# Kernel tuning notes

Measured on AMD Instinct MI355X. Metric: run time of the kernel, lower is better.

Reference implementation:

```python
import jax, jax.numpy as jnp
import numpy as np

L, V, D, S_MAX, B, S, H = 8, 32000, 1024, 1024, 4, 1024, 16
FF = 4 * D
EPS = 1e-5


def setup_inputs() -> dict:
    key = jax.random.key(0)
    ks = jax.random.split(key, 20)
    g = lambda k, shape: jax.random.normal(k, shape, dtype=jnp.float32) * 0.02
    inp = {
        'tokens': jax.random.randint(ks[0], (B, S), 0, V, dtype=jnp.int32),
        'num_heads': H,
        'emb': g(ks[1], (V, D)),
        'pos_emb': g(ks[2], (S_MAX, D)),
        'Wq': g(ks[3], (L, D, D)), 'bq': jnp.zeros((L, D), jnp.float32),
        'Wk': g(ks[4], (L, D, D)), 'bk': jnp.zeros((L, D), jnp.float32),
        'Wv': g(ks[5], (L, D, D)), 'bv': jnp.zeros((L, D), jnp.float32),
        'Wo': g(ks[6], (L, D, D)), 'bo': jnp.zeros((L, D), jnp.float32),
        'n1_s': jnp.ones((L, D), jnp.float32), 'n1_b': jnp.zeros((L, D), jnp.float32),
        'W1': g(ks[7], (L, D, FF)), 'b1': jnp.zeros((L, FF), jnp.float32),
        'W2': g(ks[8], (L, FF, D)), 'b2': jnp.zeros((L, D), jnp.float32),
        'n2_s': jnp.ones((L, D), jnp.float32), 'n2_b': jnp.zeros((L, D), jnp.float32),
    }
    return inp


def _layernorm(x, s, b):
    mu = jnp.mean(x, axis=-1, keepdims=True)
    var = jnp.mean(jnp.square(x - mu), axis=-1, keepdims=True)
    return s * (x - mu) * jax.lax.rsqrt(var + EPS) + b


def _forward(tokens, num_heads, emb, pos_emb, Wq, bq, Wk, bk, Wv, bv, Wo, bo,
             n1_s, n1_b, W1, b1, W2, b2, n2_s, n2_b):
    Bn, Sn = tokens.shape
    d = emb.shape[1]
    hd = d // num_heads
    x = emb[tokens] + pos_emb[:Sn][None, :, :]  # [B,S,D]

    def split_heads(t):  # [B,S,D] -> [B,H,S,hd]
        return t.reshape(Bn, Sn, num_heads, hd).transpose(0, 2, 1, 3)

    causal = jnp.triu(jnp.ones((Sn, Sn), dtype=bool), k=1)
    scale = 1.0 / np.sqrt(hd)
    nlayers = Wq.shape[0]
    for l in range(nlayers):
        q = split_heads(x @ Wq[l] + bq[l])
        k = split_heads(x @ Wk[l] + bk[l])
        v = split_heads(x @ Wv[l] + bv[l])
        scores = jnp.einsum('bhqd,bhkd->bhqk', q, k) * scale
        scores = jnp.where(causal, -jnp.inf, scores)
        attn = jax.nn.softmax(scores, axis=-1)
        ctx = jnp.einsum('bhqk,bhkd->bhqd', attn, v)
        ctx = ctx.transpose(0, 2, 1, 3).reshape(Bn, Sn, d)
        x = _layernorm(x + (ctx @ Wo[l] + bo[l]), n1_s[l], n1_b[l])
        h = jax.nn.relu(x @ W1[l] + b1[l])
        x = _layernorm(x + (h @ W2[l] + b2[l]), n2_s[l], n2_b[l])
    return x @ emb.T  # tied output head -> [B,S,V]


def reference(tokens, num_heads, emb, pos_emb, Wq, bq, Wk, bk, Wv, bv, Wo, bo,
              n1_s, n1_b, W1, b1, W2, b2, n2_s, n2_b):
    return _forward(tokens, num_heads, emb, pos_emb, Wq, bq, Wk, bk, Wv, bv,
                    Wo, bo, n1_s, n1_b, W1, b1, W2, b2, n2_s, n2_b)
```

## Files before the change

### kernel.cpp

```cpp
#include <hip/hip_runtime.h>

#define D_MODEL 1024
#define SEQ     1024
#define BATCH   4
#define NHEAD   16
#define HDIM    64
#define FF_DIM  4096
#define NLAYER  8
#define VOCAB   32000
#define ROWS    (BATCH*SEQ)
#define QKV_N   3072
#define LN_EPS  1e-5f

typedef __attribute__((ext_vector_type(4))) float   f32x4;
typedef __attribute__((ext_vector_type(8))) unsigned short u16x8;
typedef __attribute__((ext_vector_type(8))) __bf16  bf16x8;

typedef const unsigned int __attribute__((address_space(1)))* gas_t;
typedef unsigned int __attribute__((address_space(3)))* las_t;

__device__ __forceinline__ void gld16(const void* g, void* l) {
    __builtin_amdgcn_global_load_lds((gas_t)g, (las_t)l, 16, 0, 0);
}

__device__ __forceinline__ unsigned short f2bf(float f) {
    unsigned int u = __builtin_bit_cast(unsigned int, f);
    u += 0x7FFFu + ((u >> 16) & 1u);
    return (unsigned short)(u >> 16);
}

__device__ __forceinline__ float bf2f(unsigned short u) {
    return __builtin_bit_cast(float, (unsigned int)u << 16);
}

__device__ __forceinline__ f32x4 mfma32(u16x8 a, u16x8 b, f32x4 c) {
    return __builtin_amdgcn_mfma_f32_16x16x32_bf16(
        __builtin_bit_cast(bf16x8, a), __builtin_bit_cast(bf16x8, b), c, 0, 0, 0);
}

__global__ __launch_bounds__(256) void embed_k(
    const int* __restrict__ tok, const float* __restrict__ emb,
    const float* __restrict__ pos, float* __restrict__ x,
    unsigned short* __restrict__ xb)
{
    int bs = blockIdx.x;
    int s  = bs & (SEQ - 1);
    int tk = tok[bs];
    int c  = threadIdx.x * 4;
    float4 e = *(const float4*)(emb + (size_t)tk * D_MODEL + c);
    float4 p = *(const float4*)(pos + (size_t)s * D_MODEL + c);
    float y0 = e.x + p.x, y1 = e.y + p.y, y2 = e.z + p.z, y3 = e.w + p.w;
    size_t base = (size_t)bs * D_MODEL + c;
    *(float4*)(x + base) = make_float4(y0, y1, y2, y3);
    unsigned long long pk = (unsigned long long)f2bf(y0)
        | ((unsigned long long)f2bf(y1) << 16)
        | ((unsigned long long)f2bf(y2) << 32)
        | ((unsigned long long)f2bf(y3) << 48);
    *(unsigned long long*)(xb + base) = pk;
}

__global__ __launch_bounds__(256) void cast_bf(
    const float* __restrict__ in, unsigned short* __restrict__ out, size_t n)
{
    size_t i = ((size_t)blockIdx.x * 256 + threadIdx.x) * 4;
    if (i >= n) return;
    float4 v = *(const float4*)(in + i);
    unsigned long long pk = (unsigned long long)f2bf(v.x)
        | ((unsigned long long)f2bf(v.y) << 16)
        | ((unsigned long long)f2bf(v.z) << 32)
        | ((unsigned long long)f2bf(v.w) << 48);
    *(unsigned long long*)(out + i) = pk;
}

__global__ __launch_bounds__(256) void bias3_k(
    const float* __restrict__ bq, const float* __restrict__ bk,
    const float* __restrict__ bv, float* __restrict__ out)
{
    int l = blockIdx.x / 3, which = blockIdx.x % 3;
    const float* src = which == 0 ? bq : (which == 1 ? bk : bv);
    int i = threadIdx.x * 4;
    float4 v = *(const float4*)(src + (size_t)l * D_MODEL + i);
    *(float4*)(out + (size_t)l * QKV_N + which * D_MODEL + i) = v;
}

__device__ __forceinline__ void tc_tile(
    const float* __restrict__ W, unsigned short* __restrict__ Wt,
    int K, int N, int n0, int k0)
{
    __shared__ float t[64][65];
    int rr = threadIdx.x >> 4;
    int cc = (threadIdx.x & 15) * 4;
#pragma unroll
    for (int it = 0; it < 4; it++) {
        int r = it * 16 + rr;
        float4 v = *(const float4*)(W + (size_t)(k0 + r) * N + n0 + cc);
        t[r][cc] = v.x; t[r][cc + 1] = v.y; t[r][cc + 2] = v.z; t[r][cc + 3] = v.w;
    }
    __syncthreads();
#pragma unroll
    for (int it = 0; it < 4; it++) {
        int n = it * 16 + rr;
        unsigned long long pk = (unsigned long long)f2bf(t[cc][n])
            | ((unsigned long long)f2bf(t[cc + 1][n]) << 16)
            | ((unsigned long long)f2bf(t[cc + 2][n]) << 32)
            | ((unsigned long long)f2bf(t[cc + 3][n]) << 48);
        *(unsigned long long*)(Wt + (size_t)(n0 + n) * K + k0 + cc) = pk;
    }
}

__global__ __launch_bounds__(256) void transpose_cast(
    const float* __restrict__ W, unsigned short* __restrict__ Wt, int K, int N)
{
    tc_tile(W, Wt, K, N, blockIdx.x * 64, blockIdx.y * 64);
}

__global__ __launch_bounds__(256) void transpose_cast3(
    const float* __restrict__ Wq, const float* __restrict__ Wk,
    const float* __restrict__ Wv, unsigned short* __restrict__ Wt)
{
    const int which = blockIdx.z;
    const float* W = which == 0 ? Wq : (which == 1 ? Wk : Wv);
    tc_tile(W, Wt + (size_t)which * (1024 * 1024), 1024, 1024,
            blockIdx.x * 64, blockIdx.y * 64);
}

__global__ __launch_bounds__(256) void transpose_all(
    const float* __restrict__ Wq, const float* __restrict__ Wk,
    const float* __restrict__ Wv, const float* __restrict__ Wo,
    const float* __restrict__ W1, const float* __restrict__ W2,
    unsigned short* __restrict__ wt)
{
    int b = blockIdx.x;
    const float* W; unsigned short* out; int K, N, t;
    if (b < 768)       { int w = b >> 8; t = b & 255; W = w == 0 ? Wq : (w == 1 ? Wk : Wv);
                         out = wt + (size_t)w * 1048576; K = 1024; N = 1024; }
    else if (b < 1024) { t = b - 768;  W = Wo; out = wt + (size_t)3 * 1048576; K = 1024; N = 1024; }
    else if (b < 2048) { t = b - 1024; W = W1; out = wt + (size_t)4 * 1048576; K = 1024; N = 4096; }
    else               { t = b - 2048; W = W2; out = wt + (size_t)8 * 1048576; K = 4096; N = 1024; }
    int ntx = N >> 6;
    tc_tile(W, out, K, N, (t % ntx) * 64, (t / ntx) * 64);
}

template<int MODE>
__global__ __launch_bounds__(256, 3) void gemm_bt(
    const unsigned short* __restrict__ A, int lda,
    const unsigned short* __restrict__ Bt, int ldb,
    const float* __restrict__ bias, void* __restrict__ Cout, int N, int Klen)
{
    __shared__ unsigned short As[128 * 32];
    __shared__ unsigned short Bs[128 * 32];
    const int part = blockIdx.y;
    A  += (size_t)part * Klen;
    Bt += (size_t)part * Klen;
    int flat = blockIdx.x;
    const int bm = flat & 31, bn = flat >> 5;
    const int tid  = threadIdx.x;
    const int wid  = tid >> 6, lane = tid & 63;
    const int l16  = lane & 15, lhi = lane >> 4;
    const int wr   = wid >> 1, wc = wid & 1;

    const int srow = wid * 32 + (lane >> 2);
    const int scol = (lane & 3) * 8;
    const unsigned short* gA0 = A  + ((size_t)bm * 128 + srow) * lda + scol;
    const unsigned short* gB0 = Bt + ((size_t)bn * 128 + srow) * ldb + scol;
    unsigned short* lA = As + wid * 32 * 32;
    unsigned short* lB = Bs + wid * 32 * 32;

    f32x4 acc[4][4];
#pragma unroll
    for (int i = 0; i < 4; i++)
#pragma unroll
        for (int j = 0; j < 4; j++) acc[i][j] = (f32x4){0.f, 0.f, 0.f, 0.f};

    for (int k0 = 0; k0 < Klen; k0 += 32) {
        __syncthreads();
        gld16(gA0 + k0,                    lA);
        gld16(gA0 + k0 + 16 * (size_t)lda, lA + 16 * 32);
        gld16(gB0 + k0,                    lB);
        gld16(gB0 + k0 + 16 * (size_t)ldb, lB + 16 * 32);
        __syncthreads();
        u16x8 af[4], bfr[4];
#pragma unroll
        for (int i = 0; i < 4; i++)
            af[i] = *(const u16x8*)(As + (wr * 64 + i * 16 + l16) * 32 + lhi * 8);
#pragma unroll
        for (int i = 0; i < 4; i++)
            bfr[i] = *(const u16x8*)(Bs + (wc * 64 + i * 16 + l16) * 32 + lhi * 8);
#pragma unroll
        for (int mi = 0; mi < 4; mi++)
#pragma unroll
            for (int ni = 0; ni < 4; ni++)
                acc[mi][ni] = mfma32(af[mi], bfr[ni], acc[mi][ni]);
    }

    const size_t pofs = (size_t)part * (size_t)ROWS * N;
#pragma unroll
    for (int mi = 0; mi < 4; mi++)
#pragma unroll
        for (int ni = 0; ni < 4; ni++) {
            int row = bm * 128 + wr * 64 + mi * 16 + lhi * 4;
            int col = bn * 128 + wc * 64 + ni * 16 + l16;
            float bv = (bias && part == 0) ? bias[col] : 0.f;
#pragma unroll
            for (int j = 0; j < 4; j++) {
                float v = acc[mi][ni][j] + bv;
                size_t idx = pofs + (size_t)(row + j) * N + col;
                if constexpr (MODE == 1) {
                    ((unsigned short*)Cout)[idx] = f2bf(v);
                } else {
                    ((unsigned short*)Cout)[idx] = f2bf(v > 0.f ? v : 0.f);
                }
            }
        }
}

#define PSYNC() do { __builtin_amdgcn_s_barrier(); \
    asm volatile("s_waitcnt lgkmcnt(0)" ::: "memory"); \
    __builtin_amdgcn_sched_barrier(0); } while (0)
#define PEND() __builtin_amdgcn_s_barrier()
#define VM4()  asm volatile("s_waitcnt vmcnt(4)" ::: "memory")

#define LOADA(reg, half) do { \
    _Pragma("unroll") \
    for (int m_ = 0; m_ < 4; m_++) { \
        aF[m_][0] = *(const u16x8*)((reg) + ((half)*4 + m_) * 2048 + lane0); \
        aF[m_][1] = *(const u16x8*)((reg) + ((half)*4 + m_) * 2048 + lane1); \
    } } while (0)

#define LOADB(reg, np) do { \
    _Pragma("unroll") \
    for (int n_ = 0; n_ < 2; n_++) { \
        bF[(np)*2 + n_][0] = *(const u16x8*)((reg) + ((np)*2 + n_) * 2048 + lane0); \
        bF[(np)*2 + n_][1] = *(const u16x8*)((reg) + ((np)*2 + n_) * 2048 + lane1); \
    } } while (0)

#define MFMA8(ma, np) do { \
    __builtin_amdgcn_s_setprio(1); \
    _Pragma("unroll") \
    for (int m_ = 0; m_ < 4; m_++) \
        _Pragma("unroll") \
        for (int n_ = 0; n_ < 2; n_++) { \
            acc[(ma)+m_][(np)*2+n_] = mfma32(aF[m_][0], bF[(np)*2+n_][0], acc[(ma)+m_][(np)*2+n_]); \
            acc[(ma)+m_][(np)*2+n_] = mfma32(aF[m_][1], bF[(np)*2+n_][1], acc[(ma)+m_][(np)*2+n_]); \
        } \
    __builtin_amdgcn_s_setprio(0); \
} while (0)

template<int MODE, int SWZ>
__global__ __launch_bounds__(512, 2) void gemm256(
    const unsigned short* __restrict__ A, const unsigned short* __restrict__ Bt,
    const float* __restrict__ bias, void* __restrict__ Cout, int N, int K)
{
    __shared__ unsigned short lds[65536] __attribute__((aligned(128)));
    const int tid = threadIdx.x, wid = tid >> 6, lane = tid & 63;
    const int l16 = lane & 15, lhi = lane >> 4;
    const int wr = wid >> 2, wc = wid & 3;

    int flat = blockIdx.x;
    if constexpr (SWZ) {
        int cpx = gridDim.x >> 3; flat = (flat & 7) * cpx + (flat >> 3);
    }
    const int bm = flat & 15, bn = flat >> 4;
    const int NT = K >> 6;

    const int srowL = tid >> 3;
    const int scolb = ((tid & 7) << 4) ^ (((tid >> 3) & 7) << 4);
    const unsigned short* baseA = A  + (size_t)(bm * 256 + srowL) * K + (scolb >> 1);
    const unsigned short* baseB = Bt + (size_t)(bn * 256 + srowL) * K + (scolb >> 1);
    unsigned short* dst0 = lds + wid * 512;

    auto stage = [&](int isB, int tile, int h) {
        const unsigned short* s = (isB ? baseB : baseA) + (size_t)(h * 128) * K + (size_t)tile * 64;
        unsigned short* d = dst0 + (tile & 1) * 32768 + isB * 16384 + h * 8192;
        gld16(s, d);
        gld16(s + (size_t)64 * K, d + 4096);
    };

    const int lswz  = (l16 & 7) << 4;
    const int lane0 = ((lhi * 16) ^ lswz) + l16 * 128;
    const int lane1 = ((64 + lhi * 16) ^ lswz) + l16 * 128;

    const char* aR0 = (const char*)lds + wr * 16384;
    const char* bR0 = (const char*)lds + 32768 + (wc >> 1) * 16384 + (wc & 1) * 8192;
    const char* aR1 = aR0 + 65536;
    const char* bR1 = bR0 + 65536;

    f32x4 acc[8][4];
#pragma unroll
    for (int i = 0; i < 8; i++)
#pragma unroll
        for (int j = 0; j < 4; j++) acc[i][j] = (f32x4){0.f, 0.f, 0.f, 0.f};
    u16x8 aF[4][2], bF[4][2];

    stage(1, 0, 0); stage(1, 0, 1);
    stage(0, 0, 0); stage(0, 0, 1);
    stage(1, 1, 0); stage(1, 1, 1);
    VM4();
    __builtin_amdgcn_s_barrier();

    for (int t = 0; t < NT; t += 2) {
        const bool more = (t + 2) < NT;
        LOADA(aR0, 0); LOADB(bR0, 0); stage(0, t + 1, 0);
        PSYNC(); MFMA8(0, 0); PEND();
        LOADB(bR0, 1);                stage(0, t + 1, 1);
        PSYNC(); MFMA8(0, 1); PEND();
        LOADA(aR0, 1);                if (more) stage(1, t + 2, 0);
        PSYNC(); MFMA8(4, 0); PEND();
        if (more) { stage(1, t + 2, 1); VM4(); }
        else      { asm volatile("s_waitcnt vmcnt(0)" ::: "memory"); }
        PSYNC(); MFMA8(4, 1); PEND();
        LOADA(aR1, 0); LOADB(bR1, 0); if (more) stage(0, t + 2, 0);
        PSYNC(); MFMA8(0, 0); PEND();
        LOADB(bR1, 1);                if (more) stage(0, t + 2, 1);
        PSYNC(); MFMA8(0, 1); PEND();
        LOADA(aR1, 1);                if (more) stage(1, t + 3, 0);
        PSYNC(); MFMA8(4, 0); PEND();
        if (more) { stage(1, t + 3, 1); VM4(); }
        PSYNC(); MFMA8(4, 1); PEND();
    }

#pragma unroll
    for (int mi = 0; mi < 8; mi++)
#pragma unroll
        for (int ni = 0; ni < 4; ni++) {
            int row = bm * 256 + wr * 128 + mi * 16 + lhi * 4;
            int col = bn * 256 + wc * 64 + ni * 16 + l16;
            float bv = bias ? bias[col] : 0.f;
#pragma unroll
            for (int j = 0; j < 4; j++) {
                float v = acc[mi][ni][j] + bv;
                size_t idx = (size_t)(row + j) * N + col;
                if constexpr (MODE == 0) {
                    __builtin_nontemporal_store(v, (float*)Cout + idx);
                } else if constexpr (MODE == 1) {
                    ((unsigned short*)Cout)[idx] = f2bf(v);
                } else {
                    ((unsigned short*)Cout)[idx] = f2bf(v > 0.f ? v : 0.f);
                }
            }
        }
}

__global__ __launch_bounds__(256, 3) void attn_fwd(
    const unsigned short* __restrict__ qkv, unsigned short* __restrict__ ctxb)
{
    __shared__ unsigned short Ks[64 * 72];
    __shared__ unsigned short Vs[64 * 72];
    __shared__ unsigned short Ps[4 * 16 * 72];
    const int tid = threadIdx.x;
    const int wid = tid >> 6, lane = tid & 63;
    const int l16 = lane & 15, lhi = lane >> 4;
    const int bh  = blockIdx.y, b = bh >> 4, h = bh & 15;
    const int q0  = blockIdx.x * 64;
    const size_t rowbase = (size_t)b * SEQ;

    const int qrow = q0 + wid * 16 + l16;
    const unsigned short* qp = qkv + (rowbase + qrow) * QKV_N + h * HDIM + lhi * 8;
    u16x8 qf0 = *(const u16x8*)qp;
    u16x8 qf1 = *(const u16x8*)(qp + 32);

    f32x4 oa[4];
    float mj[4], lj[4];
#pragma unroll
    for (int i = 0; i < 4; i++) {
        oa[i] = (f32x4){0.f, 0.f, 0.f, 0.f};
        mj[i] = -1e30f; lj[i] = 0.f;
    }

    const int ntiles = blockIdx.x + 1;
    for (int kt = 0; kt < ntiles; ++kt) {
        const int kv0 = kt * 64;
        __syncthreads();
#pragma unroll
        for (int it = 0; it < 2; ++it) {
            int e = it * 256 + tid;
            int r = e >> 3, d0 = (e & 7) * 8;
            size_t goff = (rowbase + kv0 + r) * QKV_N + D_MODEL + h * HDIM + d0;
            u16x8 kk = *(const u16x8*)(qkv + goff);
            *(u16x8*)(&Ks[r * 72 + d0]) = kk;
        }
        if (tid < 128) {
            int r0 = (tid & 15) * 4, d0v = (tid >> 4) * 8;
            const unsigned short* vp = qkv + (rowbase + kv0 + r0) * QKV_N
                                       + 2 * D_MODEL + h * HDIM + d0v;
            u16x8 w0 = *(const u16x8*)vp;
            u16x8 w1 = *(const u16x8*)(vp + QKV_N);
            u16x8 w2 = *(const u16x8*)(vp + 2 * QKV_N);
            u16x8 w3 = *(const u16x8*)(vp + 3 * QKV_N);
#pragma unroll
            for (int j = 0; j < 8; j++) {
                unsigned long long pk = (unsigned long long)w0[j]
                    | ((unsigned long long)w1[j] << 16)
                    | ((unsigned long long)w2[j] << 32)
                    | ((unsigned long long)w3[j] << 48);
                *(unsigned long long*)(&Vs[(d0v + j) * 72 + r0]) = pk;
            }
        }
        __syncthreads();

        f32x4 sa[4];
#pragma unroll
        for (int ni = 0; ni < 4; ni++) {
            f32x4 z = (f32x4){0.f, 0.f, 0.f, 0.f};
            u16x8 k0f = *(const u16x8*)(&Ks[(ni * 16 + l16) * 72 + lhi * 8]);
            u16x8 k1f = *(const u16x8*)(&Ks[(ni * 16 + l16) * 72 + 32 + lhi * 8]);
            z = mfma32(qf0, k0f, z);
            z = mfma32(qf1, k1f, z);
            sa[ni] = z;
        }
        float tm[4] = {-1e30f, -1e30f, -1e30f, -1e30f};
#pragma unroll
        for (int ni = 0; ni < 4; ni++)
#pragma unroll
            for (int j = 0; j < 4; j++) {
                float v = sa[ni][j] * 0.125f;
                int row = q0 + wid * 16 + lhi * 4 + j;
                int col = kv0 + ni * 16 + l16;
                if (col > row) v = -1e30f;
                sa[ni][j] = v;
                tm[j] = fmaxf(tm[j], v);
            }
#pragma unroll
        for (int j = 0; j < 4; j++) {
#pragma unroll
            for (int off = 1; off < 16; off <<= 1)
                tm[j] = fmaxf(tm[j], __shfl_xor(tm[j], off));
        }
        float al[4], rs[4] = {0.f, 0.f, 0.f, 0.f};
#pragma unroll
        for (int j = 0; j < 4; j++) {
            float mn = fmaxf(mj[j], tm[j]);
            al[j] = __expf(mj[j] - mn);
            mj[j] = mn;
        }
#pragma unroll
        for (int ni = 0; ni < 4; ni++)
#pragma unroll
            for (int j = 0; j < 4; j++) {
                float p = __expf(sa[ni][j] - mj[j]);
                rs[j] += p;
                Ps[wid * 1152 + (lhi * 4 + j) * 72 + ni * 16 + l16] = f2bf(p);
            }
#pragma unroll
        for (int j = 0; j < 4; j++) {
#pragma unroll
            for (int off = 1; off < 16; off <<= 1)
                rs[j] += __shfl_xor(rs[j], off);
            lj[j] = lj[j] * al[j] + rs[j];
        }
#pragma unroll
        for (int di = 0; di < 4; di++)
#pragma unroll
            for (int j = 0; j < 4; j++) oa[di][j] *= al[j];
#pragma unroll
        for (int di = 0; di < 4; di++) {
#pragma unroll
            for (int kc = 0; kc < 2; kc++) {
                u16x8 pf = *(const u16x8*)(&Ps[wid * 1152 + l16 * 72 + kc * 32 + lhi * 8]);
                u16x8 vf = *(const u16x8*)(&Vs[(di * 16 + l16) * 72 + kc * 32 + lhi * 8]);
                oa[di] = mfma32(pf, vf, oa[di]);
            }
        }
    }
#pragma unroll
    for (int di = 0; di < 4; di++)
#pragma unroll
        for (int j = 0; j < 4; j++) {
            int row = q0 + wid * 16 + lhi * 4 + j;
            ctxb[(rowbase + row) * D_MODEL + h * HDIM + di * 16 + l16] =
                f2bf(oa[di][j] / lj[j]);
        }
}

__global__ __launch_bounds__(256) void ln3(
    float* __restrict__ x, const unsigned short* __restrict__ p0,
    const unsigned short* __restrict__ p1,
    const float* __restrict__ sc, const float* __restrict__ bi,
    unsigned short* __restrict__ xb)
{
    const int row = blockIdx.x;
    const int t = threadIdx.x;
    const size_t base = (size_t)row * D_MODEL + t * 4;
    float4 xv = *(const float4*)(x + base);
    ushort4 au = *(const ushort4*)(p0 + base);
    ushort4 bu = *(const ushort4*)(p1 + base);
    float v0 = xv.x + bf2f(au.x) + bf2f(bu.x);
    float v1 = xv.y + bf2f(au.y) + bf2f(bu.y);
    float v2 = xv.z + bf2f(au.z) + bf2f(bu.z);
    float v3 = xv.w + bf2f(au.w) + bf2f(bu.w);
    float sum = v0 + v1 + v2 + v3;
    float sq  = v0 * v0 + v1 * v1 + v2 * v2 + v3 * v3;
#pragma unroll
    for (int off = 1; off < 64; off <<= 1) {
        sum += __shfl_xor(sum, off);
        sq  += __shfl_xor(sq, off);
    }
    __shared__ float red[8];
    int wid = t >> 6, lane = t & 63;
    if (lane == 0) { red[wid] = sum; red[4 + wid] = sq; }
    __syncthreads();
    sum = red[0] + red[1] + red[2] + red[3];
    sq  = red[4] + red[5] + red[6] + red[7];
    float mu   = sum * (1.f / D_MODEL);
    float var  = sq * (1.f / D_MODEL) - mu * mu;
    float rstd = rsqrtf(var + LN_EPS);
    int c = t * 4;
    float4 sv = *(const float4*)(sc + c);
    float4 bv = *(const float4*)(bi + c);
    float y0 = sv.x * (v0 - mu) * rstd + bv.x;
    float y1 = sv.y * (v1 - mu) * rstd + bv.y;
    float y2 = sv.z * (v2 - mu) * rstd + bv.z;
    float y3 = sv.w * (v3 - mu) * rstd + bv.w;
    *(float4*)(x + base) = make_float4(y0, y1, y2, y3);
    unsigned long long pk = (unsigned long long)f2bf(y0)
        | ((unsigned long long)f2bf(y1) << 16)
        | ((unsigned long long)f2bf(y2) << 32)
        | ((unsigned long long)f2bf(y3) << 48);
    *(unsigned long long*)(xb + base) = pk;
}

extern "C" void kernel_launch(void* const* d_in, const int* in_sizes, int n_in,
                              void* d_out, int out_size, void* d_ws, size_t ws_size,
                              hipStream_t stream)
{
    (void)in_sizes; (void)n_in; (void)out_size;
    const int*   tokens = (const int*)d_in[0];
    const float* emb  = (const float*)d_in[2];
    const float* pose = (const float*)d_in[3];
    const float* Wq = (const float*)d_in[4];
    const float* bq = (const float*)d_in[5];
    const float* Wk = (const float*)d_in[6];
    const float* bk = (const float*)d_in[7];
    const float* Wv = (const float*)d_in[8];
    const float* bv = (const float*)d_in[9];
    const float* Wo = (const float*)d_in[10];
    const float* bo = (const float*)d_in[11];
    const float* n1s = (const float*)d_in[12];
    const float* n1b = (const float*)d_in[13];
    const float* W1 = (const float*)d_in[14];
    const float* b1 = (const float*)d_in[15];
    const float* W2 = (const float*)d_in[16];
    const float* b2 = (const float*)d_in[17];
    const float* n2s = (const float*)d_in[18];
    const float* n2b = (const float*)d_in[19];

    char* w = (char*)d_ws;
    size_t off = 0;
    auto carve = [&](size_t bytes) -> void* {
        void* p = w + off;
        off = (off + bytes + 255) & ~(size_t)255;
        return p;
    };
    float* x = (float*)carve((size_t)ROWS * D_MODEL * 4);
    unsigned short* tmp = (unsigned short*)carve((size_t)2 * ROWS * D_MODEL * 2);
    unsigned short* xb    = (unsigned short*)carve((size_t)ROWS * D_MODEL * 2);
    unsigned short* qkvb  = (unsigned short*)carve((size_t)ROWS * QKV_N * 2);
    unsigned short* cbuf  = (unsigned short*)carve((size_t)ROWS * D_MODEL * 2);
    unsigned short* hbuf  = (unsigned short*)carve((size_t)ROWS * FF_DIM * 2);
    size_t wt_off = off;
    unsigned short* wt = (unsigned short*)carve((size_t)12 * 1048576 * 2);
    float* bqkv = (float*)carve((size_t)NLAYER * QKV_N * 4);
    unsigned short* embb = qkvb;
    unsigned short* tmp1 = tmp + (size_t)ROWS * D_MODEL;
    const bool fused_t = (off <= ws_size);
    if (!fused_t) {
        off = wt_off;
        wt = (unsigned short*)carve((size_t)D_MODEL * FF_DIM * 2);
        bqkv = (float*)carve((size_t)NLAYER * QKV_N * 4);
        if (off > ws_size) return;
    }

    bias3_k<<<NLAYER * 3, 256, 0, stream>>>(bq, bk, bv, bqkv);
    embed_k<<<ROWS, 256, 0, stream>>>(tokens, emb, pose, x, xb);

    for (int l = 0; l < NLAYER; l++) {
        const float* Wq_l = Wq + (size_t)l * D_MODEL * D_MODEL;
        const float* Wk_l = Wk + (size_t)l * D_MODEL * D_MODEL;
        const float* Wv_l = Wv + (size_t)l * D_MODEL * D_MODEL;
        const float* Wo_l = Wo + (size_t)l * D_MODEL * D_MODEL;
        const float* W1_l = W1 + (size_t)l * D_MODEL * FF_DIM;
        const float* W2_l = W2 + (size_t)l * FF_DIM * D_MODEL;

        unsigned short* wtQKV = wt;
        unsigned short* wtWo  = fused_t ? wt + (size_t)3 * 1048576 : wt;
        unsigned short* wtW1  = fused_t ? wt + (size_t)4 * 1048576 : wt;
        unsigned short* wtW2  = fused_t ? wt + (size_t)8 * 1048576 : wt;

        if (fused_t) {
            transpose_all<<<3072, 256, 0, stream>>>(Wq_l, Wk_l, Wv_l, Wo_l, W1_l, W2_l, wt);
        } else {
            transpose_cast3<<<dim3(16, 16, 3), 256, 0, stream>>>(Wq_l, Wk_l, Wv_l, wtQKV);
        }
        gemm_bt<1><<<dim3(768, 1), 256, 0, stream>>>(xb, D_MODEL, wtQKV, D_MODEL,
                                                     bqkv + (size_t)l * QKV_N, qkvb, QKV_N, D_MODEL);

        attn_fwd<<<dim3(SEQ / 64, BATCH * NHEAD), 256, 0, stream>>>(qkvb, cbuf);

        if (!fused_t) transpose_cast<<<dim3(16, 16), 256, 0, stream>>>(Wo_l, wtWo, D_MODEL, D_MODEL);
        gemm_bt<1><<<dim3(256, 2), 256, 0, stream>>>(cbuf, D_MODEL, wtWo, D_MODEL,
                                                     bo + (size_t)l * D_MODEL, tmp, D_MODEL, D_MODEL / 2);
        ln3<<<ROWS, 256, 0, stream>>>(x, tmp, tmp1, n1s + (size_t)l * D_MODEL, n1b + (size_t)l * D_MODEL, xb);

        if (!fused_t) transpose_cast<<<dim3(64, 16), 256, 0, stream>>>(W1_l, wtW1, D_MODEL, FF_DIM);
        gemm256<2, 1><<<(FF_DIM / 256) * 16, 512, 0, stream>>>(xb, wtW1, b1 + (size_t)l * FF_DIM, hbuf, FF_DIM, D_MODEL);
        if (!fused_t) transpose_cast<<<dim3(16, 64), 256, 0, stream>>>(W2_l, wtW2, FF_DIM, D_MODEL);
        gemm_bt<1><<<dim3(256, 2), 256, 0, stream>>>(hbuf, FF_DIM, wtW2, FF_DIM,
                                                     b2 + (size_t)l * D_MODEL, tmp, D_MODEL, FF_DIM / 2);
        ln3<<<ROWS, 256, 0, stream>>>(x, tmp, tmp1, n2s + (size_t)l * D_MODEL, n2b + (size_t)l * D_MODEL, xb);
    }

    cast_bf<<<(VOCAB * D_MODEL) / 1024, 256, 0, stream>>>(emb, embb, (size_t)VOCAB * D_MODEL);
    gemm256<0, 0><<<(VOCAB / 256) * 16, 512, 0, stream>>>(xb, embb, nullptr, d_out, VOCAB, D_MODEL);
}
```

Before: 2.272 ms.

## Pair causal attention query tiles per block to balance work and share K/V loads

```diff
diff --git a/kernel.cpp b/kernel.cpp
--- a/kernel.cpp
+++ b/kernel.cpp
@@ -351,24 +351,97 @@
     const int wid = tid >> 6, lane = tid & 63;
     const int l16 = lane & 15, lhi = lane >> 4;
     const int bh  = blockIdx.y, b = bh >> 4, h = bh & 15;
-    const int q0  = blockIdx.x * 64;
+    const int p   = blockIdx.x;
+    const int qA0 = p * 64;
+    const int qB0 = (15 - p) * 64;
     const size_t rowbase = (size_t)b * SEQ;
 
-    const int qrow = q0 + wid * 16 + l16;
-    const unsigned short* qp = qkv + (rowbase + qrow) * QKV_N + h * HDIM + lhi * 8;
-    u16x8 qf0 = *(const u16x8*)qp;
-    u16x8 qf1 = *(const u16x8*)(qp + 32);
-
-    f32x4 oa[4];
-    float mj[4], lj[4];
+    const unsigned short* qpA = qkv + (rowbase + qA0 + wid * 16 + l16) * QKV_N + h * HDIM + lhi * 8;
+    u16x8 qAf0 = *(const u16x8*)qpA;
+    u16x8 qAf1 = *(const u16x8*)(qpA + 32);
+    const unsigned short* qpB = qkv + (rowbase + qB0 + wid * 16 + l16) * QKV_N + h * HDIM + lhi * 8;
+    u16x8 qBf0 = *(const u16x8*)qpB;
+    u16x8 qBf1 = *(const u16x8*)(qpB + 32);
+
+    f32x4 oaA[4], oaB[4];
+    float mjA[4], ljA[4], mjB[4], ljB[4];
 #pragma unroll
     for (int i = 0; i < 4; i++) {
-        oa[i] = (f32x4){0.f, 0.f, 0.f, 0.f};
-        mj[i] = -1e30f; lj[i] = 0.f;
-    }
-
-    const int ntiles = blockIdx.x + 1;
-    for (int kt = 0; kt < ntiles; ++kt) {
+        oaA[i] = (f32x4){0.f, 0.f, 0.f, 0.f};
+        oaB[i] = (f32x4){0.f, 0.f, 0.f, 0.f};
+        mjA[i] = -1e30f; ljA[i] = 0.f;
+        mjB[i] = -1e30f; ljB[i] = 0.f;
+    }
+
+    auto update = [&](u16x8 qf0, u16x8 qf1, f32x4 (&oa)[4],
+                      float (&mj)[4], float (&lj)[4], int q0, int kv0) {
+        f32x4 sa[4];
+#pragma unroll
+        for (int ni = 0; ni < 4; ni++) {
+            f32x4 z = (f32x4){0.f, 0.f, 0.f, 0.f};
+            u16x8 k0f = *(const u16x8*)(&Ks[(ni * 16 + l16) * 72 + lhi * 8]);
+            u16x8 k1f = *(const u16x8*)(&Ks[(ni * 16 + l16) * 72 + 32 + lhi * 8]);
+            z = mfma32(qf0, k0f, z);
+            z = mfma32(qf1, k1f, z);
+            sa[ni] = z;
+        }
+        float tm[4] = {-1e30f, -1e30f, -1e30f, -1e30f};
+#pragma unroll
+        for (int ni = 0; ni < 4; ni++)
+#pragma unroll
+            for (int j = 0; j < 4; j++) {
+                float v = sa[ni][j] * 0.125f;
+                int row = q0 + wid * 16 + lhi * 4 + j;
+                int col = kv0 + ni * 16 + l16;
+                if (col > row) v = -1e30f;
+                sa[ni][j] = v;
+                tm[j] = fmaxf(tm[j], v);
+            }
+#pragma unroll
+        for (int j = 0; j < 4; j++) {
+#pragma unroll
+            for (int off = 1; off < 16; off <<= 1)
+                tm[j] = fmaxf(tm[j], __shfl_xor(tm[j], off));
+        }
+        float al[4], rs[4] = {0.f, 0.f, 0.f, 0.f};
+#pragma unroll
+        for (int j = 0; j < 4; j++) {
+            float mn = fmaxf(mj[j], tm[j]);
+            al[j] = __expf(mj[j] - mn);
+            mj[j] = mn;
+        }
+#pragma unroll
+        for (int ni = 0; ni < 4; ni++)
+#pragma unroll
+            for (int j = 0; j < 4; j++) {
+                float pv = __expf(sa[ni][j] - mj[j]);
+                rs[j] += pv;
+                Ps[wid * 1152 + (lhi * 4 + j) * 72 + ni * 16 + l16] = f2bf(pv);
+            }
+#pragma unroll
+        for (int j = 0; j < 4; j++) {
+#pragma unroll
+            for (int off = 1; off < 16; off <<= 1)
+                rs[j] += __shfl_xor(rs[j], off);
+            lj[j] = lj[j] * al[j] + rs[j];
+        }
+#pragma unroll
+        for (int di = 0; di < 4; di++)
+#pragma unroll
+            for (int j = 0; j < 4; j++) oa[di][j] *= al[j];
+#pragma unroll
+        for (int di = 0; di < 4; di++) {
+#pragma unroll
+            for (int kc = 0; kc < 2; kc++) {
+                u16x8 pf = *(const u16x8*)(&Ps[wid * 1152 + l16 * 72 + kc * 32 + lhi * 8]);
+                u16x8 vf = *(const u16x8*)(&Vs[(di * 16 + l16) * 72 + kc * 32 + lhi * 8]);
+                oa[di] = mfma32(pf, vf, oa[di]);
+            }
+        }
+    };
+
+    const int ntB = 16 - p;
+    for (int kt = 0; kt < ntB; ++kt) {
         const int kv0 = kt * 64;
         __syncthreads();
 #pragma unroll
@@ -398,77 +471,20 @@
         }
         __syncthreads();
 
-        f32x4 sa[4];
-#pragma unroll
-        for (int ni = 0; ni < 4; ni++) {
-            f32x4 z = (f32x4){0.f, 0.f, 0.f, 0.f};
-            u16x8 k0f = *(const u16x8*)(&Ks[(ni * 16 + l16) * 72 + lhi * 8]);
-            u16x8 k1f = *(const u16x8*)(&Ks[(ni * 16 + l16) * 72 + 32 + lhi * 8]);
-            z = mfma32(qf0, k0f, z);
-            z = mfma32(qf1, k1f, z);
-            sa[ni] = z;
-        }
-        float tm[4] = {-1e30f, -1e30f, -1e30f, -1e30f};
-#pragma unroll
-        for (int ni = 0; ni < 4; ni++)
-#pragma unroll
-            for (int j = 0; j < 4; j++) {
-                float v = sa[ni][j] * 0.125f;
-                int row = q0 + wid * 16 + lhi * 4 + j;
-                int col = kv0 + ni * 16 + l16;
-                if (col > row) v = -1e30f;
-                sa[ni][j] = v;
-                tm[j] = fmaxf(tm[j], v);
-            }
+        if (kt <= p) update(qAf0, qAf1, oaA, mjA, ljA, qA0, kv0);
+        update(qBf0, qBf1, oaB, mjB, ljB, qB0, kv0);
+    }
+
+#pragma unroll
+    for (int di = 0; di < 4; di++)
 #pragma unroll
         for (int j = 0; j < 4; j++) {
-#pragma unroll
-            for (int off = 1; off < 16; off <<= 1)
-                tm[j] = fmaxf(tm[j], __shfl_xor(tm[j], off));
-        }
-        float al[4], rs[4] = {0.f, 0.f, 0.f, 0.f};
-#pragma unroll
-        for (int j = 0; j < 4; j++) {
-            float mn = fmaxf(mj[j], tm[j]);
-            al[j] = __expf(mj[j] - mn);
-            mj[j] = mn;
-        }
-#pragma unroll
-        for (int ni = 0; ni < 4; ni++)
-#pragma unroll
-            for (int j = 0; j < 4; j++) {
-                float p = __expf(sa[ni][j] - mj[j]);
-                rs[j] += p;
-                Ps[wid * 1152 + (lhi * 4 + j) * 72 + ni * 16 + l16] = f2bf(p);
-            }
-#pragma unroll
-        for (int j = 0; j < 4; j++) {
-#pragma unroll
-            for (int off = 1; off < 16; off <<= 1)
-                rs[j] += __shfl_xor(rs[j], off);
-            lj[j] = lj[j] * al[j] + rs[j];
-        }
-#pragma unroll
-        for (int di = 0; di < 4; di++)
-#pragma unroll
-            for (int j = 0; j < 4; j++) oa[di][j] *= al[j];
-#pragma unroll
-        for (int di = 0; di < 4; di++) {
-#pragma unroll
-            for (int kc = 0; kc < 2; kc++) {
-                u16x8 pf = *(const u16x8*)(&Ps[wid * 1152 + l16 * 72 + kc * 32 + lhi * 8]);
-                u16x8 vf = *(const u16x8*)(&Vs[(di * 16 + l16) * 72 + kc * 32 + lhi * 8]);
-                oa[di] = mfma32(pf, vf, oa[di]);
-            }
-        }
-    }
-#pragma unroll
-    for (int di = 0; di < 4; di++)
-#pragma unroll
-        for (int j = 0; j < 4; j++) {
-            int row = q0 + wid * 16 + lhi * 4 + j;
-            ctxb[(rowbase + row) * D_MODEL + h * HDIM + di * 16 + l16] =
-                f2bf(oa[di][j] / lj[j]);
+            int rowA = qA0 + wid * 16 + lhi * 4 + j;
+            ctxb[(rowbase + rowA) * D_MODEL + h * HDIM + di * 16 + l16] =
+                f2bf(oaA[di][j] / ljA[j]);
+            int rowB = qB0 + wid * 16 + lhi * 4 + j;
+            ctxb[(rowbase + rowB) * D_MODEL + h * HDIM + di * 16 + l16] =
+                f2bf(oaB[di][j] / ljB[j]);
         }
 }
 
@@ -594,7 +610,7 @@
         gemm_bt<1><<<dim3(768, 1), 256, 0, stream>>>(xb, D_MODEL, wtQKV, D_MODEL,
                                                      bqkv + (size_t)l * QKV_N, qkvb, QKV_N, D_MODEL);
 
-        attn_fwd<<<dim3(SEQ / 64, BATCH * NHEAD), 256, 0, stream>>>(qkvb, cbuf);
+        attn_fwd<<<dim3(8, BATCH * NHEAD), 256, 0, stream>>>(qkvb, cbuf);
 
         if (!fused_t) transpose_cast<<<dim3(16, 16), 256, 0, stream>>>(Wo_l, wtWo, D_MODEL, D_MODEL);
         gemm_bt<1><<<dim3(256, 2), 256, 0, stream>>>(cbuf, D_MODEL, wtWo, D_MODEL,
```

After: 2.159 ms. 4.9% less time.
